# Kernel optimization log

Hardware: AMD Instinct MI355X
Metric: run time of the kernel (lower is better)

Reference implementation:

```python
import jax, jax.numpy as jnp
import numpy as np

DIM = 1024
HEADS = 16
HEAD_DIM = DIM // HEADS
B, N, S = 4, 4096, 512


def setup_inputs() -> dict:
    key = jax.random.key(0)
    ks = jax.random.split(key, 9)
    scale = DIM ** -0.5
    return {
        "x": jax.random.normal(ks[0], (B, N, DIM), dtype=jnp.float32),
        "context": jax.random.normal(ks[1], (B, S, DIM), dtype=jnp.float32),
        "context_mask": jax.random.uniform(ks[2], (B, S)) < 0.2,  # True = padding
        "q_w": jax.random.normal(ks[3], (DIM, DIM), dtype=jnp.float32) * scale,
        "q_b": jnp.zeros((DIM,), dtype=jnp.float32),
        "kv_w": jax.random.normal(ks[4], (DIM, 2 * DIM), dtype=jnp.float32) * scale,
        "kv_b": jnp.zeros((2 * DIM,), dtype=jnp.float32),
        "proj_w": jax.random.normal(ks[5], (DIM, DIM), dtype=jnp.float32) * scale,
        "proj_b": jnp.zeros((DIM,), dtype=jnp.float32),
    }


def reference(x, context, context_mask, q_w, q_b, kv_w, kv_b, proj_w, proj_b):
    b, n, c = x.shape
    s = context.shape[1]
    h, d = HEADS, HEAD_DIM
    scale = d ** -0.5

    # projections
    q = (x @ q_w + q_b).reshape(b, n, h, d)            # [B,N,H,D]
    kv = (context @ kv_w + kv_b).reshape(b, s, 2, h, d)
    k = kv[:, :, 0]                                     # [B,S,H,D]
    v = kv[:, :, 1]

    # scores [B,H,N,S]
    attn = jnp.einsum("bnhd,bshd->bhns", q, k) * scale
    attn = jnp.where(context_mask[:, None, None, :], -jnp.inf, attn)
    attn = jax.nn.softmax(attn, axis=-1)

    out = jnp.einsum("bhns,bshd->bnhd", attn, v).reshape(b, n, c)
    return out @ proj_w + proj_b
```

## Files before the change

kernel.cpp:

```cpp
#include <hip/hip_runtime.h>
#include <hip/hip_bf16.h>

typedef __attribute__((ext_vector_type(8))) short bf16x8;
typedef __attribute__((ext_vector_type(4))) float f32x4;
typedef unsigned short u16;

#define DIMC 1024
#define NHEAD 16
#define HDIM 64
#define NB 4
#define NQ 4096
#define NS 512

#define LOG2E 1.44269504f

#if __has_builtin(__builtin_amdgcn_exp2f)
#define EXP2F(x) __builtin_amdgcn_exp2f(x)
#else
#define EXP2F(x) __expf(0.69314718f * (x))
#endif

#if __has_builtin(__builtin_amdgcn_rcpf)
#define RCPF(x) __builtin_amdgcn_rcpf(x)
#else
#define RCPF(x) (1.0f / (x))
#endif

__device__ __forceinline__ u16 f2bf(float f) {
  __hip_bfloat16 h = __float2bfloat16(f);
  return *reinterpret_cast<u16*>(&h);
}

__device__ __forceinline__ unsigned pack_bf2(float a, float b) {
  __hip_bfloat162 h2 = __float22bfloat162_rn(make_float2(a, b));
  return *reinterpret_cast<unsigned*>(&h2);
}

__device__ __forceinline__ void gload_lds16(const void* g, void* s) {
  __builtin_amdgcn_global_load_lds(
      (const __attribute__((address_space(1))) void*)g,
      (__attribute__((address_space(3))) void*)s, 16, 0, 0);
}


__device__ __forceinline__ void cvt_body(const float* __restrict__ in,
                                         u16* __restrict__ out, int base, int nblk,
                                         int n4) {
  const int stride = nblk * 256;
  for (int i = base * 256 + threadIdx.x; i < n4; i += stride) {
    float4 v = *(const float4*)(in + (size_t)i * 4);
    ushort4 o;
    o.x = f2bf(v.x); o.y = f2bf(v.y); o.z = f2bf(v.z); o.w = f2bf(v.w);
    *(ushort4*)(out + (size_t)i * 4) = o;
  }
}

__global__ void prep_kernel(const float* __restrict__ x, const float* __restrict__ ctx,
                            const int* __restrict__ cmask,
                            const float* __restrict__ q_w, const float* __restrict__ kv_w,
                            const float* __restrict__ proj_w,
                            u16* __restrict__ x_bf, u16* __restrict__ ctx_bf,
                            u16* __restrict__ qwT, u16* __restrict__ kvwT,
                            u16* __restrict__ pwT, float* __restrict__ maskf) {
  __shared__ float t[32][33];
  const int bid = blockIdx.x;
  if (bid < 2048) {
    cvt_body(x, x_bf, bid, 2048, 16777216 / 4);
    return;
  }
  if (bid < 2560) {
    cvt_body(ctx, ctx_bf, bid - 2048, 512, 2097152 / 4);
    return;
  }
  if (bid >= 6656) {
    const int i = (bid - 6656) * 256 + threadIdx.x;
    if (i < NB * NS) maskf[i] = cmask[i] ? -1e30f : 0.0f;
    return;
  }
  const float* W;
  u16* WT;
  int K, N, local;
  if (bid < 3584) {
    W = q_w; WT = qwT; K = 1024; N = 1024; local = bid - 2560;
  } else if (bid < 5632) {
    W = kv_w; WT = kvwT; K = 1024; N = 2048; local = bid - 3584;
  } else {
    W = proj_w; WT = pwT; K = 1024; N = 1024; local = bid - 5632;
  }
  const int nbx = N >> 5;
  const int bx = (local % nbx) * 32;
  const int by = (local / nbx) * 32;
  const int tx = threadIdx.x & 31, ty = threadIdx.x >> 5;
#pragma unroll
  for (int i = 0; i < 32; i += 8)
    t[ty + i][tx] = W[(size_t)(by + ty + i) * N + bx + tx];
  __syncthreads();
#pragma unroll
  for (int i = 0; i < 32; i += 8)
    WT[(size_t)(bx + ty + i) * K + by + tx] = f2bf(t[tx][ty + i]);
}


__launch_bounds__(256)
__global__ void gemm_kv(const u16* __restrict__ A, const u16* __restrict__ BT,
                        const float* __restrict__ bias, u16* __restrict__ Kout,
                        u16* __restrict__ VTout, int M, int N, int K) {
  __shared__ __align__(16) u16 As[128 * 32];
  __shared__ __align__(16) u16 Bs[128 * 32];
  const int tid = threadIdx.x;
  const int w = tid >> 6, l = tid & 63;
  const int wr = w >> 1, wc = w & 1;
  const int fr = l & 15, fhi = l >> 4;

  const int nwg = gridDim.x * gridDim.y;
  const int o = blockIdx.y * gridDim.x + blockIdx.x;
  const int tIdx = (o & 7) * (nwg >> 3) + (o >> 3);
  const int m0 = (tIdx / gridDim.x) * 128;
  const int n0 = (tIdx % gridDim.x) * 128;

  const f32x4 fz = {0.f, 0.f, 0.f, 0.f};
  f32x4 acc[4][4];
#pragma unroll
  for (int mt = 0; mt < 4; mt++)
#pragma unroll
    for (int nt = 0; nt < 4; nt++) acc[mt][nt] = fz;

  const int f0 = w * 2048 + l * 16;
  const int f1 = f0 + 1024;
  const int ar0 = f0 >> 6, ac0 = (f0 & 63) >> 1;
  const int ar1 = f1 >> 6, ac1 = (f1 & 63) >> 1;
  const u16* Ag0 = A + (size_t)(m0 + ar0) * K + ac0;
  const u16* Ag1 = A + (size_t)(m0 + ar1) * K + ac1;
  const u16* Bg0 = BT + (size_t)(n0 + ar0) * K + ac0;
  const u16* Bg1 = BT + (size_t)(n0 + ar1) * K + ac1;

  for (int k0 = 0; k0 < K; k0 += 32) {
    gload_lds16(Ag0 + k0, &As[w * 1024]);
    gload_lds16(Ag1 + k0, &As[w * 1024 + 512]);
    gload_lds16(Bg0 + k0, &Bs[w * 1024]);
    gload_lds16(Bg1 + k0, &Bs[w * 1024 + 512]);
    __syncthreads();

    bf16x8 a[4], b[4];
#pragma unroll
    for (int t = 0; t < 4; t++) {
      a[t] = *(const bf16x8*)&As[(wr * 64 + t * 16 + fr) * 32 + fhi * 8];
      b[t] = *(const bf16x8*)&Bs[(wc * 64 + t * 16 + fr) * 32 + fhi * 8];
    }
#pragma unroll
    for (int mt = 0; mt < 4; mt++)
#pragma unroll
      for (int nt = 0; nt < 4; nt++)
        acc[mt][nt] = __builtin_amdgcn_mfma_f32_16x16x32_bf16(a[mt], b[nt], acc[mt][nt], 0, 0, 0);
    __syncthreads();
  }

#pragma unroll
  for (int mt = 0; mt < 4; mt++) {
#pragma unroll
    for (int nt = 0; nt < 4; nt++) {
      const int col = n0 + wc * 64 + nt * 16 + fr;
      const float bv = bias[col];
#pragma unroll
      for (int r = 0; r < 4; r++) {
        const int row = m0 + wr * 64 + mt * 16 + fhi * 4 + r;
        const float v = acc[mt][nt][r] + bv;
        const int b = row >> 9, s = row & 511;
        if (col < 1024) {
          const int h = col >> 6, d = col & 63;
          Kout[(((size_t)(b * 16 + h)) * 512 + s) * 64 + d] = f2bf(v);
        } else {
          const int c2 = col - 1024;
          const int h = c2 >> 6, d = c2 & 63;
          VTout[(((size_t)(b * 16 + h)) * 64 + d) * 512 + s] = f2bf(v);
        }
      }
    }
  }
}


template<int MODE>
__launch_bounds__(512, 1)
__global__ void gemm256(const u16* __restrict__ A, const u16* __restrict__ BT,
                        const float* __restrict__ bias, void* __restrict__ C0,
                        int M, int N, int K) {
  __shared__ __align__(16) u16 As[2][16384];
  __shared__ __align__(16) u16 Bs[2][16384];
  const int tid = threadIdx.x;
  const int w = tid >> 6, l = tid & 63;
  const int wm = w >> 2, wn = w & 3;
  const int fr = l & 15, fhi = l >> 4;

  const int nblk = gridDim.x;
  const int nN = N >> 8;
  const int o = blockIdx.x;
  const int tIdx = (o & 7) * (nblk >> 3) + (o >> 3);
  const int m0 = (tIdx / nN) << 8;
  const int n0 = (tIdx % nN) << 8;

  const int rowoff = tid >> 3;
  const int gchunk = (tid & 7) ^ (rowoff & 7);
  const u16* Abase = A + (size_t)(m0 + rowoff) * K + gchunk * 8;
  const u16* Bbase = BT + (size_t)(n0 + rowoff) * K + gchunk * 8;
  const int ldsoff = w * 512;

  const f32x4 fz = {0.f, 0.f, 0.f, 0.f};
  f32x4 acc[2][4][4];
#pragma unroll
  for (int mh = 0; mh < 2; mh++)
#pragma unroll
    for (int m = 0; m < 4; m++)
#pragma unroll
      for (int n = 0; n < 4; n++) acc[mh][m][n] = fz;

  const int KT = K >> 6;

#pragma unroll
  for (int p = 0; p < 4; ++p) {
    gload_lds16(Abase + (size_t)(p * 64) * K, &As[0][p * 4096 + ldsoff]);
    gload_lds16(Bbase + (size_t)(p * 64) * K, &Bs[0][p * 4096 + ldsoff]);
  }
  asm volatile("s_waitcnt vmcnt(0)" ::: "memory");
  __builtin_amdgcn_s_barrier();

  int nb = 0;
  for (int kt = 0; kt < KT; ++kt) {
    const int knext = (kt + 1) << 6;
    const bool more = (kt + 1) < KT;
#pragma unroll
    for (int p = 0; p < 4; ++p) {
      const int mh = p >> 1, kk = p & 1;
      const int ch = ((kk << 2) | fhi) ^ (fr & 7);
      bf16x8 af[4], bfr[4];
#pragma unroll
      for (int m = 0; m < 4; ++m) {
        const int row = wm * 128 + mh * 64 + m * 16 + fr;
        af[m] = *(const bf16x8*)((const char*)&As[nb][0] + row * 128 + ch * 16);
      }
#pragma unroll
      for (int n = 0; n < 4; ++n) {
        const int row = wn * 64 + n * 16 + fr;
        bfr[n] = *(const bf16x8*)((const char*)&Bs[nb][0] + row * 128 + ch * 16);
      }
      if (more) {
        gload_lds16(Abase + (size_t)(p * 64) * K + knext, &As[nb ^ 1][p * 4096 + ldsoff]);
        gload_lds16(Bbase + (size_t)(p * 64) * K + knext, &Bs[nb ^ 1][p * 4096 + ldsoff]);
      }
      __builtin_amdgcn_s_barrier();
      asm volatile("s_waitcnt lgkmcnt(0)" ::: "memory");
      __builtin_amdgcn_s_setprio(1);
#pragma unroll
      for (int m = 0; m < 4; ++m)
#pragma unroll
        for (int n = 0; n < 4; ++n)
          acc[mh][m][n] = __builtin_amdgcn_mfma_f32_16x16x32_bf16(af[m], bfr[n], acc[mh][m][n], 0, 0, 0);
      __builtin_amdgcn_s_setprio(0);
      __builtin_amdgcn_s_barrier();
    }
    asm volatile("s_waitcnt vmcnt(0)" ::: "memory");
    __builtin_amdgcn_s_barrier();
    nb ^= 1;
  }

#pragma unroll
  for (int mh = 0; mh < 2; ++mh)
#pragma unroll
    for (int m = 0; m < 4; ++m)
#pragma unroll
      for (int n = 0; n < 4; ++n) {
        const int col = n0 + wn * 64 + n * 16 + fr;
        const float bv = bias[col];
#pragma unroll
        for (int r = 0; r < 4; ++r) {
          const int row = m0 + wm * 128 + mh * 64 + m * 16 + fhi * 4 + r;
          const float v = acc[mh][m][n][r] + bv;
          if (MODE == 0)
            ((u16*)C0)[(size_t)row * N + col] = f2bf(v * 0.125f);
          else
            ((float*)C0)[(size_t)row * N + col] = v;
        }
      }
}

__launch_bounds__(512, 2)
__global__ void attn_kernel(const u16* __restrict__ Q, const u16* __restrict__ Kb,
                            const u16* __restrict__ VT, const float* __restrict__ maskf,
                            u16* __restrict__ O) {
  __shared__ __align__(16) u16 Ks[512 * 64];
  __shared__ __align__(16) u16 Vs[64 * 512];
  __shared__ __align__(16) u16 Ps[8][2048];
  const int tid = threadIdx.x, w = tid >> 6, l = tid & 63;
  const int fr = l & 15, fhi = l >> 4;

  const int rid = blockIdx.x;
  const int orig = ((rid & 7) << 6) + (rid >> 3);
  const int bh = orig >> 3, qc = orig & 7;
  const int b = bh >> 4, h = bh & 15;

  const u16* Kg = Kb + (size_t)bh * NS * HDIM;
  const u16* Vg = VT + (size_t)bh * HDIM * NS;
  const float* mrow = maskf + b * NS;

#pragma unroll
  for (int it = 0; it < 8; ++it) {
    const int slot = it * 512 + tid;
    const int r = slot >> 3, c3 = slot & 7;
    const int gc = c3 ^ (r & 7);
    gload_lds16(Kg + (size_t)r * HDIM + gc * 8, &Ks[slot * 8]);
  }
#pragma unroll
  for (int it = 0; it < 8; ++it) {
    const int slot = it * 512 + tid;
    const int r = slot >> 6, c6 = slot & 63;
    const int gc = c6 ^ (r & 7);
    gload_lds16(Vg + (size_t)r * NS + gc * 8, &Vs[slot * 8]);
  }
  asm volatile("s_waitcnt vmcnt(0)" ::: "memory");
  __syncthreads();

  u16* Pw = Ps[w];
  const f32x4 fz = {0.f, 0.f, 0.f, 0.f};

  const int rowbase_a = b * NQ + qc * 512 + w * 64;
  const int rowbase_b = rowbase_a + 32;

  bf16x8 qfa[2][2], qfb[2][2];
#pragma unroll
  for (int mt = 0; mt < 2; mt++)
#pragma unroll
    for (int kk = 0; kk < 2; kk++) {
      qfa[mt][kk] = *(const bf16x8*)&Q[(size_t)(rowbase_a + mt * 16 + fr) * DIMC +
                                       h * 64 + kk * 32 + fhi * 8];
      qfb[mt][kk] = *(const bf16x8*)&Q[(size_t)(rowbase_b + mt * 16 + fr) * DIMC +
                                       h * 64 + kk * 32 + fhi * 8];
    }

  float l_a[2] = {0.f, 0.f}, l_b[2] = {0.f, 0.f};
  f32x4 oa[2][4], ob[2][4];
#pragma unroll
  for (int mt = 0; mt < 2; mt++)
#pragma unroll
    for (int dn = 0; dn < 4; dn++) { oa[mt][dn] = fz; ob[mt][dn] = fz; }

#pragma unroll
  for (int t = 0; t < 8; ++t) {
    const int sc = t * 64;

    float4 mv4[4];
#pragma unroll
    for (int sn = 0; sn < 4; sn++)
      mv4[sn] = *(const float4*)&mrow[sc + sn * 16 + fhi * 4];

    f32x4 sa[2][4];
#pragma unroll
    for (int mt = 0; mt < 2; mt++)
#pragma unroll
      for (int sn = 0; sn < 4; sn++) sa[mt][sn] = fz;
    __builtin_amdgcn_s_setprio(1);
#pragma unroll
    for (int kk = 0; kk < 2; kk++) {
      bf16x8 kf[4];
#pragma unroll
      for (int sn = 0; sn < 4; sn++) {
        const int row = sc + sn * 16 + fr;
        const int byte = row * 128 + ((((kk << 2) | fhi) ^ (fr & 7)) << 4);
        kf[sn] = *(const bf16x8*)((const char*)&Ks[0] + byte);
      }
#pragma unroll
      for (int sn = 0; sn < 4; sn++)
#pragma unroll
        for (int mt = 0; mt < 2; mt++)
          sa[mt][sn] = __builtin_amdgcn_mfma_f32_16x16x32_bf16(kf[sn], qfa[mt][kk], sa[mt][sn], 0, 0, 0);
    }
    __builtin_amdgcn_s_setprio(0);

#pragma unroll
    for (int mt = 0; mt < 2; mt++) {
      float ls = 0.f;
      const int qrow = mt * 16 + fr;
#pragma unroll
      for (int sn = 0; sn < 4; sn++) {
        const float e0 = EXP2F(fmaf(sa[mt][sn][0], LOG2E, ((const float*)&mv4[sn])[0]));
        const float e1 = EXP2F(fmaf(sa[mt][sn][1], LOG2E, ((const float*)&mv4[sn])[1]));
        const float e2 = EXP2F(fmaf(sa[mt][sn][2], LOG2E, ((const float*)&mv4[sn])[2]));
        const float e3 = EXP2F(fmaf(sa[mt][sn][3], LOG2E, ((const float*)&mv4[sn])[3]));
        ls += (e0 + e1) + (e2 + e3);
        int byte = qrow * 128 + sn * 32 + fhi * 8;
        byte ^= (qrow & 7) << 4;
        uint2 pk;
        pk.x = pack_bf2(e0, e1);
        pk.y = pack_bf2(e2, e3);
        *(uint2*)((char*)Pw + byte) = pk;
      }
      l_a[mt] += ls;
    }

    f32x4 sb[2][4];
#pragma unroll
    for (int mt = 0; mt < 2; mt++)
#pragma unroll
      for (int sn = 0; sn < 4; sn++) sb[mt][sn] = fz;
    __builtin_amdgcn_s_setprio(1);
#pragma unroll
    for (int kk = 0; kk < 2; kk++) {
      bf16x8 kf[4];
#pragma unroll
      for (int sn = 0; sn < 4; sn++) {
        const int row = sc + sn * 16 + fr;
        const int byte = row * 128 + ((((kk << 2) | fhi) ^ (fr & 7)) << 4);
        kf[sn] = *(const bf16x8*)((const char*)&Ks[0] + byte);
      }
#pragma unroll
      for (int sn = 0; sn < 4; sn++)
#pragma unroll
        for (int mt = 0; mt < 2; mt++)
          sb[mt][sn] = __builtin_amdgcn_mfma_f32_16x16x32_bf16(kf[sn], qfb[mt][kk], sb[mt][sn], 0, 0, 0);
    }
    __builtin_amdgcn_s_setprio(0);

    asm volatile("s_waitcnt lgkmcnt(0)" ::: "memory");
    __builtin_amdgcn_s_setprio(1);
#pragma unroll
    for (int kk = 0; kk < 2; kk++) {
      bf16x8 vv[4];
#pragma unroll
      for (int dn = 0; dn < 4; dn++) {
        const int row = dn * 16 + fr;
        const int byte = row * 1024 +
            (((sc >> 3) + ((((kk << 2) | fhi) ^ (fr & 7)))) << 4);
        vv[dn] = *(const bf16x8*)((const char*)&Vs[0] + byte);
      }
#pragma unroll
      for (int mt = 0; mt < 2; mt++) {
        int byte = (mt * 16 + fr) * 128 + kk * 64 + fhi * 16;
        byte ^= (fr & 7) << 4;
        const bf16x8 pa = *(const bf16x8*)((char*)Pw + byte);
#pragma unroll
        for (int dn = 0; dn < 4; dn++)
          oa[mt][dn] = __builtin_amdgcn_mfma_f32_16x16x32_bf16(pa, vv[dn], oa[mt][dn], 0, 0, 0);
      }
    }
    __builtin_amdgcn_s_setprio(0);

#pragma unroll
    for (int mt = 0; mt < 2; mt++) {
      float ls = 0.f;
      const int qrow = mt * 16 + fr;
#pragma unroll
      for (int sn = 0; sn < 4; sn++) {
        const float e0 = EXP2F(fmaf(sb[mt][sn][0], LOG2E, ((const float*)&mv4[sn])[0]));
        const float e1 = EXP2F(fmaf(sb[mt][sn][1], LOG2E, ((const float*)&mv4[sn])[1]));
        const float e2 = EXP2F(fmaf(sb[mt][sn][2], LOG2E, ((const float*)&mv4[sn])[2]));
        const float e3 = EXP2F(fmaf(sb[mt][sn][3], LOG2E, ((const float*)&mv4[sn])[3]));
        ls += (e0 + e1) + (e2 + e3);
        int byte = qrow * 128 + sn * 32 + fhi * 8;
        byte ^= (qrow & 7) << 4;
        uint2 pk;
        pk.x = pack_bf2(e0, e1);
        pk.y = pack_bf2(e2, e3);
        *(uint2*)((char*)Pw + byte) = pk;
      }
      l_b[mt] += ls;
    }

    asm volatile("s_waitcnt lgkmcnt(0)" ::: "memory");
    __builtin_amdgcn_s_setprio(1);
#pragma unroll
    for (int kk = 0; kk < 2; kk++) {
      bf16x8 vv[4];
#pragma unroll
      for (int dn = 0; dn < 4; dn++) {
        const int row = dn * 16 + fr;
        const int byte = row * 1024 +
            (((sc >> 3) + ((((kk << 2) | fhi) ^ (fr & 7)))) << 4);
        vv[dn] = *(const bf16x8*)((const char*)&Vs[0] + byte);
      }
#pragma unroll
      for (int mt = 0; mt < 2; mt++) {
        int byte = (mt * 16 + fr) * 128 + kk * 64 + fhi * 16;
        byte ^= (fr & 7) << 4;
        const bf16x8 pa = *(const bf16x8*)((char*)Pw + byte);
#pragma unroll
        for (int dn = 0; dn < 4; dn++)
          ob[mt][dn] = __builtin_amdgcn_mfma_f32_16x16x32_bf16(pa, vv[dn], ob[mt][dn], 0, 0, 0);
      }
    }
    __builtin_amdgcn_s_setprio(0);
  }

#pragma unroll
  for (int mt = 0; mt < 2; mt++) {
    l_a[mt] += __shfl_xor(l_a[mt], 16);
    l_a[mt] += __shfl_xor(l_a[mt], 32);
    l_b[mt] += __shfl_xor(l_b[mt], 16);
    l_b[mt] += __shfl_xor(l_b[mt], 32);
  }
#pragma unroll
  for (int mt = 0; mt < 2; mt++) {
    float loa[4], lob[4];
#pragma unroll
    for (int r = 0; r < 4; r++) {
      loa[r] = RCPF(__shfl(l_a[mt], fhi * 4 + r));
      lob[r] = RCPF(__shfl(l_b[mt], fhi * 4 + r));
    }
#pragma unroll
    for (int dn = 0; dn < 4; dn++)
#pragma unroll
      for (int r = 0; r < 4; r++) {
        const int rowa = rowbase_a + mt * 16 + fhi * 4 + r;
        O[(size_t)rowa * DIMC + h * 64 + dn * 16 + fr] = f2bf(oa[mt][dn][r] * loa[r]);
        const int rowb = rowbase_b + mt * 16 + fhi * 4 + r;
        O[(size_t)rowb * DIMC + h * 64 + dn * 16 + fr] = f2bf(ob[mt][dn][r] * lob[r]);
      }
  }
}


extern "C" void kernel_launch(void* const* d_in, const int* in_sizes, int n_in,
                              void* d_out, int out_size, void* d_ws, size_t ws_size,
                              hipStream_t stream) {
  const float* x      = (const float*)d_in[0];
  const float* ctx    = (const float*)d_in[1];
  const int*   cmask  = (const int*)d_in[2];
  const float* q_w    = (const float*)d_in[3];
  const float* q_b    = (const float*)d_in[4];
  const float* kv_w   = (const float*)d_in[5];
  const float* kv_b   = (const float*)d_in[6];
  const float* proj_w = (const float*)d_in[7];
  const float* proj_b = (const float*)d_in[8];
  float* out = (float*)d_out;

  char* ws = (char*)d_ws;
  size_t off = 0;
  auto alloc = [&](size_t bytes) {
    void* p = ws + off;
    off += (bytes + 255) & ~(size_t)255;
    return p;
  };
  u16* x_bf   = (u16*)alloc((size_t)16384 * 1024 * 2);
  u16* ctx_bf = (u16*)alloc((size_t)2048 * 1024 * 2);
  u16* qwT    = (u16*)alloc((size_t)1024 * 1024 * 2);
  u16* kvwT   = (u16*)alloc((size_t)2048 * 1024 * 2);
  u16* pwT    = (u16*)alloc((size_t)1024 * 1024 * 2);
  u16* Qb     = (u16*)alloc((size_t)16384 * 1024 * 2);
  u16* Kbuf   = (u16*)alloc((size_t)64 * 512 * 64 * 2);
  u16* VTbuf  = (u16*)alloc((size_t)64 * 64 * 512 * 2);
  u16* Ob     = (u16*)alloc((size_t)16384 * 1024 * 2);
  float* maskf = (float*)alloc((size_t)NB * NS * 4);

  prep_kernel<<<6664, 256, 0, stream>>>(x, ctx, cmask, q_w, kv_w, proj_w,
                                        x_bf, ctx_bf, qwT, kvwT, pwT, maskf);

  gemm256<0><<<256, 512, 0, stream>>>(x_bf, qwT, q_b, Qb, 16384, 1024, 1024);
  gemm_kv<<<dim3(16, 16), 256, 0, stream>>>(ctx_bf, kvwT, kv_b, Kbuf, VTbuf, 2048, 2048, 1024);
  attn_kernel<<<512, 512, 0, stream>>>(Qb, Kbuf, VTbuf, maskf, Ob);
  gemm256<2><<<256, 512, 0, stream>>>(Ob, pwT, proj_b, out, 16384, 1024, 1024);
}
```

Measured before the change: 184.8 us.

## Halve attention grid, loop two query tiles per block, row sums via MFMA

The attention kernel now launches 256 blocks, and each block processes 1024 query rows in two passes. The K/V tiles staged in LDS are therefore reused across twice as many queries, which halves the global K/V loads and LDS fills. K and V fragments are loaded once per step and shared between the two half-tiles. The softmax denominator is now computed by an extra MFMA against a vector of ones instead of scalar adds and cross-lane shuffles. This adds MFMA work and uses the bf16-rounded P values in the sum, and 256 blocks may underfill the 256-CU device at 2 blocks per CU.

```diff
diff --git a/kernel.cpp b/kernel.cpp
--- a/kernel.cpp
+++ b/kernel.cpp
@@ -294,8 +294,8 @@
   const int fr = l & 15, fhi = l >> 4;
 
   const int rid = blockIdx.x;
-  const int orig = ((rid & 7) << 6) + (rid >> 3);
-  const int bh = orig >> 3, qc = orig & 7;
+  const int orig = ((rid & 7) << 5) + (rid >> 3);
+  const int bh = orig >> 2, qc = orig & 3;
   const int b = bh >> 4, h = bh & 15;
 
   const u16* Kg = Kb + (size_t)bh * NS * HDIM;
@@ -322,197 +322,182 @@
   u16* Pw = Ps[w];
   const f32x4 fz = {0.f, 0.f, 0.f, 0.f};
 
-  const int rowbase_a = b * NQ + qc * 512 + w * 64;
-  const int rowbase_b = rowbase_a + 32;
-
-  bf16x8 qfa[2][2], qfb[2][2];
-#pragma unroll
-  for (int mt = 0; mt < 2; mt++)
-#pragma unroll
-    for (int kk = 0; kk < 2; kk++) {
-      qfa[mt][kk] = *(const bf16x8*)&Q[(size_t)(rowbase_a + mt * 16 + fr) * DIMC +
-                                       h * 64 + kk * 32 + fhi * 8];
-      qfb[mt][kk] = *(const bf16x8*)&Q[(size_t)(rowbase_b + mt * 16 + fr) * DIMC +
-                                       h * 64 + kk * 32 + fhi * 8];
+  bf16x8 onesf;
+#pragma unroll
+  for (int i = 0; i < 8; ++i) onesf[i] = (short)0x3F80;
+
+#pragma unroll 1
+  for (int qt2 = 0; qt2 < 2; ++qt2) {
+    const int rowbase_a = b * NQ + qc * 1024 + w * 128 + qt2 * 64;
+    const int rowbase_b = rowbase_a + 32;
+
+    bf16x8 qfa[2][2], qfb[2][2];
+#pragma unroll
+    for (int mt = 0; mt < 2; mt++)
+#pragma unroll
+      for (int kk = 0; kk < 2; kk++) {
+        qfa[mt][kk] = *(const bf16x8*)&Q[(size_t)(rowbase_a + mt * 16 + fr) * DIMC +
+                                         h * 64 + kk * 32 + fhi * 8];
+        qfb[mt][kk] = *(const bf16x8*)&Q[(size_t)(rowbase_b + mt * 16 + fr) * DIMC +
+                                         h * 64 + kk * 32 + fhi * 8];
+      }
+
+    f32x4 lacc_a[2], lacc_b[2];
+    f32x4 oa[2][4], ob[2][4];
+#pragma unroll
+    for (int mt = 0; mt < 2; mt++) {
+      lacc_a[mt] = fz; lacc_b[mt] = fz;
+#pragma unroll
+      for (int dn = 0; dn < 4; dn++) { oa[mt][dn] = fz; ob[mt][dn] = fz; }
     }
 
-  float l_a[2] = {0.f, 0.f}, l_b[2] = {0.f, 0.f};
-  f32x4 oa[2][4], ob[2][4];
-#pragma unroll
-  for (int mt = 0; mt < 2; mt++)
-#pragma unroll
-    for (int dn = 0; dn < 4; dn++) { oa[mt][dn] = fz; ob[mt][dn] = fz; }
-
-#pragma unroll
-  for (int t = 0; t < 8; ++t) {
-    const int sc = t * 64;
-
-    float4 mv4[4];
-#pragma unroll
-    for (int sn = 0; sn < 4; sn++)
-      mv4[sn] = *(const float4*)&mrow[sc + sn * 16 + fhi * 4];
-
-    f32x4 sa[2][4];
-#pragma unroll
-    for (int mt = 0; mt < 2; mt++)
-#pragma unroll
-      for (int sn = 0; sn < 4; sn++) sa[mt][sn] = fz;
-    __builtin_amdgcn_s_setprio(1);
-#pragma unroll
-    for (int kk = 0; kk < 2; kk++) {
-      bf16x8 kf[4];
-#pragma unroll
-      for (int sn = 0; sn < 4; sn++) {
-        const int row = sc + sn * 16 + fr;
-        const int byte = row * 128 + ((((kk << 2) | fhi) ^ (fr & 7)) << 4);
-        kf[sn] = *(const bf16x8*)((const char*)&Ks[0] + byte);
-      }
+#pragma unroll
+    for (int t = 0; t < 8; ++t) {
+      const int sc = t * 64;
+
+      bf16x8 kf[2][4];
+#pragma unroll
+      for (int kk = 0; kk < 2; kk++)
+#pragma unroll
+        for (int sn = 0; sn < 4; sn++) {
+          const int row = sc + sn * 16 + fr;
+          const int byte = row * 128 + ((((kk << 2) | fhi) ^ (fr & 7)) << 4);
+          kf[kk][sn] = *(const bf16x8*)((const char*)&Ks[0] + byte);
+        }
+
+      f32x4 sa[2][4];
+#pragma unroll
+      for (int mt = 0; mt < 2; mt++)
+#pragma unroll
+        for (int sn = 0; sn < 4; sn++) sa[mt][sn] = fz;
+      __builtin_amdgcn_s_setprio(1);
+#pragma unroll
+      for (int kk = 0; kk < 2; kk++)
+#pragma unroll
+        for (int sn = 0; sn < 4; sn++)
+#pragma unroll
+          for (int mt = 0; mt < 2; mt++)
+            sa[mt][sn] = __builtin_amdgcn_mfma_f32_16x16x32_bf16(kf[kk][sn], qfa[mt][kk], sa[mt][sn], 0, 0, 0);
+      __builtin_amdgcn_s_setprio(0);
+
+      float4 mv4[4];
 #pragma unroll
       for (int sn = 0; sn < 4; sn++)
-#pragma unroll
-        for (int mt = 0; mt < 2; mt++)
-          sa[mt][sn] = __builtin_amdgcn_mfma_f32_16x16x32_bf16(kf[sn], qfa[mt][kk], sa[mt][sn], 0, 0, 0);
+        mv4[sn] = *(const float4*)&mrow[sc + sn * 16 + fhi * 4];
+
+#pragma unroll
+      for (int mt = 0; mt < 2; mt++) {
+        const int qrow = mt * 16 + fr;
+#pragma unroll
+        for (int sn = 0; sn < 4; sn++) {
+          const float e0 = EXP2F(fmaf(sa[mt][sn][0], LOG2E, ((const float*)&mv4[sn])[0]));
+          const float e1 = EXP2F(fmaf(sa[mt][sn][1], LOG2E, ((const float*)&mv4[sn])[1]));
+          const float e2 = EXP2F(fmaf(sa[mt][sn][2], LOG2E, ((const float*)&mv4[sn])[2]));
+          const float e3 = EXP2F(fmaf(sa[mt][sn][3], LOG2E, ((const float*)&mv4[sn])[3]));
+          int byte = qrow * 128 + sn * 32 + fhi * 8;
+          byte ^= (qrow & 7) << 4;
+          uint2 pk;
+          pk.x = pack_bf2(e0, e1);
+          pk.y = pack_bf2(e2, e3);
+          *(uint2*)((char*)Pw + byte) = pk;
+        }
+      }
+      asm volatile("s_waitcnt lgkmcnt(0)" ::: "memory");
+
+      bf16x8 vv[2][4];
+#pragma unroll
+      for (int kk = 0; kk < 2; kk++)
+#pragma unroll
+        for (int dn = 0; dn < 4; dn++) {
+          const int row = dn * 16 + fr;
+          const int byte = row * 1024 +
+              (((sc >> 3) + ((((kk << 2) | fhi) ^ (fr & 7)))) << 4);
+          vv[kk][dn] = *(const bf16x8*)((const char*)&Vs[0] + byte);
+        }
+
+      __builtin_amdgcn_s_setprio(1);
+#pragma unroll
+      for (int kk = 0; kk < 2; kk++)
+#pragma unroll
+        for (int mt = 0; mt < 2; mt++) {
+          int byte = (mt * 16 + fr) * 128 + kk * 64 + fhi * 16;
+          byte ^= (fr & 7) << 4;
+          const bf16x8 pa = *(const bf16x8*)((char*)Pw + byte);
+#pragma unroll
+          for (int dn = 0; dn < 4; dn++)
+            oa[mt][dn] = __builtin_amdgcn_mfma_f32_16x16x32_bf16(pa, vv[kk][dn], oa[mt][dn], 0, 0, 0);
+          lacc_a[mt] = __builtin_amdgcn_mfma_f32_16x16x32_bf16(pa, onesf, lacc_a[mt], 0, 0, 0);
+        }
+      __builtin_amdgcn_s_setprio(0);
+
+      f32x4 sb[2][4];
+#pragma unroll
+      for (int mt = 0; mt < 2; mt++)
+#pragma unroll
+        for (int sn = 0; sn < 4; sn++) sb[mt][sn] = fz;
+      __builtin_amdgcn_s_setprio(1);
+#pragma unroll
+      for (int kk = 0; kk < 2; kk++)
+#pragma unroll
+        for (int sn = 0; sn < 4; sn++)
+#pragma unroll
+          for (int mt = 0; mt < 2; mt++)
+            sb[mt][sn] = __builtin_amdgcn_mfma_f32_16x16x32_bf16(kf[kk][sn], qfb[mt][kk], sb[mt][sn], 0, 0, 0);
+      __builtin_amdgcn_s_setprio(0);
+
+#pragma unroll
+      for (int mt = 0; mt < 2; mt++) {
+        const int qrow = mt * 16 + fr;
+#pragma unroll
+        for (int sn = 0; sn < 4; sn++) {
+          const float e0 = EXP2F(fmaf(sb[mt][sn][0], LOG2E, ((const float*)&mv4[sn])[0]));
+          const float e1 = EXP2F(fmaf(sb[mt][sn][1], LOG2E, ((const float*)&mv4[sn])[1]));
+          const float e2 = EXP2F(fmaf(sb[mt][sn][2], LOG2E, ((const float*)&mv4[sn])[2]));
+          const float e3 = EXP2F(fmaf(sb[mt][sn][3], LOG2E, ((const float*)&mv4[sn])[3]));
+          int byte = qrow * 128 + sn * 32 + fhi * 8;
+          byte ^= (qrow & 7) << 4;
+          uint2 pk;
+          pk.x = pack_bf2(e0, e1);
+          pk.y = pack_bf2(e2, e3);
+          *(uint2*)((char*)Pw + byte) = pk;
+        }
+      }
+      asm volatile("s_waitcnt lgkmcnt(0)" ::: "memory");
+
+      __builtin_amdgcn_s_setprio(1);
+#pragma unroll
+      for (int kk = 0; kk < 2; kk++)
+#pragma unroll
+        for (int mt = 0; mt < 2; mt++) {
+          int byte = (mt * 16 + fr) * 128 + kk * 64 + fhi * 16;
+          byte ^= (fr & 7) << 4;
+          const bf16x8 pa = *(const bf16x8*)((char*)Pw + byte);
+#pragma unroll
+          for (int dn = 0; dn < 4; dn++)
+            ob[mt][dn] = __builtin_amdgcn_mfma_f32_16x16x32_bf16(pa, vv[kk][dn], ob[mt][dn], 0, 0, 0);
+          lacc_b[mt] = __builtin_amdgcn_mfma_f32_16x16x32_bf16(pa, onesf, lacc_b[mt], 0, 0, 0);
+        }
+      __builtin_amdgcn_s_setprio(0);
     }
-    __builtin_amdgcn_s_setprio(0);
 
 #pragma unroll
     for (int mt = 0; mt < 2; mt++) {
-      float ls = 0.f;
-      const int qrow = mt * 16 + fr;
-#pragma unroll
-      for (int sn = 0; sn < 4; sn++) {
-        const float e0 = EXP2F(fmaf(sa[mt][sn][0], LOG2E, ((const float*)&mv4[sn])[0]));
-        const float e1 = EXP2F(fmaf(sa[mt][sn][1], LOG2E, ((const float*)&mv4[sn])[1]));
-        const float e2 = EXP2F(fmaf(sa[mt][sn][2], LOG2E, ((const float*)&mv4[sn])[2]));
-        const float e3 = EXP2F(fmaf(sa[mt][sn][3], LOG2E, ((const float*)&mv4[sn])[3]));
-        ls += (e0 + e1) + (e2 + e3);
-        int byte = qrow * 128 + sn * 32 + fhi * 8;
-        byte ^= (qrow & 7) << 4;
-        uint2 pk;
-        pk.x = pack_bf2(e0, e1);
-        pk.y = pack_bf2(e2, e3);
-        *(uint2*)((char*)Pw + byte) = pk;
-      }
-      l_a[mt] += ls;
+      float loa[4], lob[4];
+#pragma unroll
+      for (int r = 0; r < 4; r++) {
+        loa[r] = RCPF(lacc_a[mt][r]);
+        lob[r] = RCPF(lacc_b[mt][r]);
+      }
+#pragma unroll
+      for (int dn = 0; dn < 4; dn++)
+#pragma unroll
+        for (int r = 0; r < 4; r++) {
+          const int rowa = rowbase_a + mt * 16 + fhi * 4 + r;
+          O[(size_t)rowa * DIMC + h * 64 + dn * 16 + fr] = f2bf(oa[mt][dn][r] * loa[r]);
+          const int rowb = rowbase_b + mt * 16 + fhi * 4 + r;
+          O[(size_t)rowb * DIMC + h * 64 + dn * 16 + fr] = f2bf(ob[mt][dn][r] * lob[r]);
+        }
     }
-
-    f32x4 sb[2][4];
-#pragma unroll
-    for (int mt = 0; mt < 2; mt++)
-#pragma unroll
-      for (int sn = 0; sn < 4; sn++) sb[mt][sn] = fz;
-    __builtin_amdgcn_s_setprio(1);
-#pragma unroll
-    for (int kk = 0; kk < 2; kk++) {
-      bf16x8 kf[4];
-#pragma unroll
-      for (int sn = 0; sn < 4; sn++) {
-        const int row = sc + sn * 16 + fr;
-        const int byte = row * 128 + ((((kk << 2) | fhi) ^ (fr & 7)) << 4);
-        kf[sn] = *(const bf16x8*)((const char*)&Ks[0] + byte);
-      }
-#pragma unroll
-      for (int sn = 0; sn < 4; sn++)
-#pragma unroll
-        for (int mt = 0; mt < 2; mt++)
-          sb[mt][sn] = __builtin_amdgcn_mfma_f32_16x16x32_bf16(kf[sn], qfb[mt][kk], sb[mt][sn], 0, 0, 0);
-    }
-    __builtin_amdgcn_s_setprio(0);
-
-    asm volatile("s_waitcnt lgkmcnt(0)" ::: "memory");
-    __builtin_amdgcn_s_setprio(1);
-#pragma unroll
-    for (int kk = 0; kk < 2; kk++) {
-      bf16x8 vv[4];
-#pragma unroll
-      for (int dn = 0; dn < 4; dn++) {
-        const int row = dn * 16 + fr;
-        const int byte = row * 1024 +
-            (((sc >> 3) + ((((kk << 2) | fhi) ^ (fr & 7)))) << 4);
-        vv[dn] = *(const bf16x8*)((const char*)&Vs[0] + byte);
-      }
-#pragma unroll
-      for (int mt = 0; mt < 2; mt++) {
-        int byte = (mt * 16 + fr) * 128 + kk * 64 + fhi * 16;
-        byte ^= (fr & 7) << 4;
-        const bf16x8 pa = *(const bf16x8*)((char*)Pw + byte);
-#pragma unroll
-        for (int dn = 0; dn < 4; dn++)
-          oa[mt][dn] = __builtin_amdgcn_mfma_f32_16x16x32_bf16(pa, vv[dn], oa[mt][dn], 0, 0, 0);
-      }
-    }
-    __builtin_amdgcn_s_setprio(0);
-
-#pragma unroll
-    for (int mt = 0; mt < 2; mt++) {
-      float ls = 0.f;
-      const int qrow = mt * 16 + fr;
-#pragma unroll
-      for (int sn = 0; sn < 4; sn++) {
-        const float e0 = EXP2F(fmaf(sb[mt][sn][0], LOG2E, ((const float*)&mv4[sn])[0]));
-        const float e1 = EXP2F(fmaf(sb[mt][sn][1], LOG2E, ((const float*)&mv4[sn])[1]));
-        const float e2 = EXP2F(fmaf(sb[mt][sn][2], LOG2E, ((const float*)&mv4[sn])[2]));
-        const float e3 = EXP2F(fmaf(sb[mt][sn][3], LOG2E, ((const float*)&mv4[sn])[3]));
-        ls += (e0 + e1) + (e2 + e3);
-        int byte = qrow * 128 + sn * 32 + fhi * 8;
-        byte ^= (qrow & 7) << 4;
-        uint2 pk;
-        pk.x = pack_bf2(e0, e1);
-        pk.y = pack_bf2(e2, e3);
-        *(uint2*)((char*)Pw + byte) = pk;
-      }
-      l_b[mt] += ls;
-    }
-
-    asm volatile("s_waitcnt lgkmcnt(0)" ::: "memory");
-    __builtin_amdgcn_s_setprio(1);
-#pragma unroll
-    for (int kk = 0; kk < 2; kk++) {
-      bf16x8 vv[4];
-#pragma unroll
-      for (int dn = 0; dn < 4; dn++) {
-        const int row = dn * 16 + fr;
-        const int byte = row * 1024 +
-            (((sc >> 3) + ((((kk << 2) | fhi) ^ (fr & 7)))) << 4);
-        vv[dn] = *(const bf16x8*)((const char*)&Vs[0] + byte);
-      }
-#pragma unroll
-      for (int mt = 0; mt < 2; mt++) {
-        int byte = (mt * 16 + fr) * 128 + kk * 64 + fhi * 16;
-        byte ^= (fr & 7) << 4;
-        const bf16x8 pa = *(const bf16x8*)((char*)Pw + byte);
-#pragma unroll
-        for (int dn = 0; dn < 4; dn++)
-          ob[mt][dn] = __builtin_amdgcn_mfma_f32_16x16x32_bf16(pa, vv[dn], ob[mt][dn], 0, 0, 0);
-      }
-    }
-    __builtin_amdgcn_s_setprio(0);
-  }
-
-#pragma unroll
-  for (int mt = 0; mt < 2; mt++) {
-    l_a[mt] += __shfl_xor(l_a[mt], 16);
-    l_a[mt] += __shfl_xor(l_a[mt], 32);
-    l_b[mt] += __shfl_xor(l_b[mt], 16);
-    l_b[mt] += __shfl_xor(l_b[mt], 32);
-  }
-#pragma unroll
-  for (int mt = 0; mt < 2; mt++) {
-    float loa[4], lob[4];
-#pragma unroll
-    for (int r = 0; r < 4; r++) {
-      loa[r] = RCPF(__shfl(l_a[mt], fhi * 4 + r));
-      lob[r] = RCPF(__shfl(l_b[mt], fhi * 4 + r));
-    }
-#pragma unroll
-    for (int dn = 0; dn < 4; dn++)
-#pragma unroll
-      for (int r = 0; r < 4; r++) {
-        const int rowa = rowbase_a + mt * 16 + fhi * 4 + r;
-        O[(size_t)rowa * DIMC + h * 64 + dn * 16 + fr] = f2bf(oa[mt][dn][r] * loa[r]);
-        const int rowb = rowbase_b + mt * 16 + fhi * 4 + r;
-        O[(size_t)rowb * DIMC + h * 64 + dn * 16 + fr] = f2bf(ob[mt][dn][r] * lob[r]);
-      }
   }
 }
 
@@ -554,6 +539,6 @@
 
   gemm256<0><<<256, 512, 0, stream>>>(x_bf, qwT, q_b, Qb, 16384, 1024, 1024);
   gemm_kv<<<dim3(16, 16), 256, 0, stream>>>(ctx_bf, kvwT, kv_b, Kbuf, VTbuf, 2048, 2048, 1024);
-  attn_kernel<<<512, 512, 0, stream>>>(Qb, Kbuf, VTbuf, maskf, Ob);
+  attn_kernel<<<256, 512, 0, stream>>>(Qb, Kbuf, VTbuf, maskf, Ob);
   gemm256<2><<<256, 512, 0, stream>>>(Ob, pwT, proj_b, out, 16384, 1024, 1024);
 }
```

After: 177.2 us. -4.2%, faster.
